# Optimization experiments

Measured on AMD Instinct MI355X. Metric: run time of the kernel, lower is better.

Reference implementation:

```python
import jax, jax.numpy as jnp
import numpy as np

CUTOFF = 5.0
CUTOFF_ANGLE = 3.5
N = 25000
E = 800000
EA = 300000
T = 1600000
NBASIS = 8          # default radial basis size (bessel)
NBASIS_ANG = 8
DIM = 256
DIM_SRC = 64
DIM_DST = 32
DIM_ANGLE = 8
NMAX_ANGLE = 4
SPECIES_DIM = 16
NSPEC = 50


def bessel_basis(r, rc, n):
    # sin(k*pi*r/rc)/r Bessel-type radial basis, k=1..n  -> [E, n]
    x = r[:, None]
    k = jnp.arange(1, n + 1, dtype=r.dtype)[None, :] * (np.pi / rc)
    return jnp.sqrt(2.0 / rc) * jnp.sin(k * x) / x


def tssr2(x):
    # two-sided smooth square-root activation (identity inside |x|<=1)
    ax = jnp.abs(x)
    return jnp.where(ax <= 1.0, x, jnp.sign(x) * (2.0 * jnp.sqrt(jnp.maximum(ax, 1.0)) - 1.0))


def setup_inputs() -> dict:
    key = jax.random.key(0)
    ks = jax.random.split(key, 24)
    species = jax.random.randint(ks[0], (N,), 1, 17)
    edge_src = jax.random.randint(ks[1], (E,), 0, N)
    edge_dst = jax.random.randint(ks[2], (E,), 0, N)
    distances = 0.5 + jax.random.uniform(ks[3], (E,)) * (CUTOFF - 0.5)
    switch = 0.5 + 0.5 * jnp.cos(np.pi * distances / CUTOFF)
    angles = jax.random.uniform(ks[4], (T,)) * np.pi
    angle_src = jax.random.randint(ks[5], (T,), 0, EA)
    angle_dst = jax.random.randint(ks[6], (T,), 0, EA)
    central_atom = jax.random.randint(ks[7], (T,), 0, N)
    distances_angle = 0.5 + jax.random.uniform(ks[8], (EA,)) * (CUTOFF_ANGLE - 0.5)
    switch_angle = 0.5 + 0.5 * jnp.cos(np.pi * distances_angle / CUTOFF_ANGLE)
    s = lambda k, sh, scale: jax.random.normal(k, sh, jnp.float32) * scale
    din0 = SPECIES_DIM + DIM_SRC + NBASIS * DIM_DST + (NMAX_ANGLE + 1) * DIM_ANGLE  # 376
    din1 = DIM + DIM_SRC + NBASIS * DIM_DST + (NMAX_ANGLE + 1) * DIM_ANGLE          # 616
    return {
        'species': species, 'edge_src': edge_src, 'edge_dst': edge_dst,
        'distances': distances, 'switch': switch,
        'angles': angles, 'angle_src': angle_src, 'angle_dst': angle_dst,
        'central_atom': central_atom, 'distances_angle': distances_angle,
        'switch_angle': switch_angle,
        'species_table': s(ks[9], (NSPEC, SPECIES_DIM), 1.0),
        'W_si0': s(ks[10], (SPECIES_DIM, DIM_SRC + DIM_DST), SPECIES_DIM ** -0.5),
        'W_si1': s(ks[11], (DIM, DIM_SRC + DIM_DST), DIM ** -0.5),
        'W_da0': s(ks[12], (NBASIS_ANG, DIM_ANGLE), NBASIS_ANG ** -0.5),
        'W_da1': s(ks[13], (NBASIS_ANG, DIM_ANGLE), NBASIS_ANG ** -0.5),
        'W_mix0': s(ks[14], (din0, DIM), din0 ** -0.5),
        'b_mix0': jnp.zeros((DIM,), jnp.float32),
        'W_mix1': s(ks[15], (din1, DIM), din1 ** -0.5),
        'b_mix1': jnp.zeros((DIM,), jnp.float32),
    }


def reference(species, edge_src, edge_dst, distances, switch, angles, angle_src,
              angle_dst, central_atom, distances_angle, switch_angle,
              species_table, W_si0, W_si1, W_da0, W_da1,
              W_mix0, b_mix0, W_mix1, b_mix1):
    n_atoms = species.shape[0]
    # species encoding (learned/random table lookup)
    xi = species_table[species]                                   # [N, 16]
    # radial embeddings, smoothly switched at cutoff
    rb = bessel_basis(distances, CUTOFF, NBASIS) * switch[:, None]            # [E, 8]
    rba = bessel_basis(distances_angle, CUTOFF_ANGLE, NBASIS_ANG) * switch_angle[:, None]  # [EA, 8]
    # fourier angular features cos(n*theta), n=0..nmax_angle
    nvec = jnp.arange(NMAX_ANGLE + 1, dtype=angles.dtype)[None, :]
    xa = jnp.cos(nvec * angles[:, None])                          # [T, 5]
    for W_si, W_da, W_mix, b_mix in ((W_si0, W_da0, W_mix0, b_mix0),
                                     (W_si1, W_da1, W_mix1, b_mix1)):
        s = xi @ W_si                                             # [N, 96]
        si, si_dst = s[:, :DIM_SRC], s[:, DIM_SRC:]
        # radial message passing: outer(radial_basis, neighbor features) -> scatter-add
        mij = (rb[:, :, None] * si_dst[edge_dst][:, None, :]).reshape(rb.shape[0], -1)  # [E, 256]
        mi = jax.ops.segment_sum(mij, edge_src, num_segments=n_atoms)                   # [N, 256]
        # angular triplet features: pairwise vectors combined per angle
        da = rba @ W_da                                           # [EA, 8]
        dij = da[angle_src] * da[angle_dst]                       # [T, 8]
        ang = (xa[:, :, None] * dij[:, None, :]).reshape(xa.shape[0], -1)               # [T, 40]
        ami = jax.ops.segment_sum(ang, central_atom, num_segments=n_atoms)              # [N, 40]
        # mixing network + tssr2 mixing activation, residual when shapes match
        ei = jnp.concatenate([xi, si, mi, ami], axis=-1)
        dxi = tssr2(ei @ W_mix + b_mix)
        xi = xi + dxi if xi.shape[-1] == dxi.shape[-1] else dxi
    return xi
```

## Files before the change

kernel.cpp:

```cpp
#include <hip/hip_runtime.h>
#include <hip/hip_bf16.h>

typedef __hip_bfloat16 bf16;
typedef __bf16 bf8 __attribute__((ext_vector_type(8)));
typedef float  f4  __attribute__((ext_vector_type(4)));

#define N_ATOMS 25000
#define NE      800000
#define NEA     300000
#define NT      1600000
#define APB     64
#define NBUK    ((N_ATOMS + APB - 1) / APB)

#define DIN0  376
#define DIN1  616
#define DINP0 384
#define DINP1 640

#define EBLK ((NE + 4095) / 4096)

__device__ __forceinline__ float tssr2f(float x) {
    float ax = fabsf(x);
    return (ax <= 1.f) ? x : copysignf(2.f * __builtin_sqrtf(ax) - 1.f, x);
}

__device__ __forceinline__ unsigned short f2bf_rn(float v) {
    unsigned int b = __float_as_uint(v);
    b += 0x7FFF + ((b >> 16) & 1);
    return (unsigned short)(b >> 16);
}
__device__ __forceinline__ float bf2f(unsigned short u) {
    return __uint_as_float(((unsigned int)u) << 16);
}

__global__ __launch_bounds__(256) void k_bcount(const int* __restrict__ esrc,
                                                const int* __restrict__ cat,
                                                int* __restrict__ ebcnt,
                                                int* __restrict__ tbcnt) {
    __shared__ int h[NBUK];
    int t = threadIdx.x;
    for (int b = t; b < NBUK; b += 256) h[b] = 0;
    __syncthreads();
    bool isE = blockIdx.x < EBLK;
    const int* key = isE ? esrc : cat;
    int n = isE ? NE : NT;
    int base = (isE ? blockIdx.x : (blockIdx.x - EBLK)) * 4096;
#pragma unroll
    for (int k = 0; k < 16; k++) {
        int idx = base + k * 256 + t;
        if (idx < n) atomicAdd(&h[key[idx] >> 6], 1);
    }
    __syncthreads();
    int* g = isE ? ebcnt : tbcnt;
    for (int b = t; b < NBUK; b += 256)
        if (h[b]) atomicAdd(&g[b], h[b]);
}

__global__ __launch_bounds__(512) void k_scanB(const int* cnt0, int* off0, int* cur0,
                                               int* aoff0,
                                               const int* cnt1, int* off1, int* cur1,
                                               int* aoff1) {
    const int* cnt = blockIdx.x ? cnt1 : cnt0;
    int* off  = blockIdx.x ? off1 : off0;
    int* cur  = blockIdx.x ? cur1 : cur0;
    int* aoff = blockIdx.x ? aoff1 : aoff0;
    int nelem = blockIdx.x ? NT : NE;
    __shared__ int sh[512];
    int t = threadIdx.x;
    int v = (t < NBUK) ? cnt[t] : 0;
    sh[t] = v;
    __syncthreads();
    for (int d = 1; d < 512; d <<= 1) {
        int a = (t >= d) ? sh[t - d] : 0;
        __syncthreads();
        sh[t] += a;
        __syncthreads();
    }
    int excl = sh[t] - v;
    if (t <= NBUK) { off[t] = excl; if (t < NBUK) cur[t] = excl; }
    if (t == 0) aoff[N_ATOMS] = nelem;
}

template <bool EDGE>
__global__ __launch_bounds__(512) void k_binA(const float* __restrict__ fA,
                                              const float* __restrict__ fB,
                                              const int* __restrict__ iB,
                                              const int* __restrict__ iC,
                                              const int* __restrict__ key,
                                              int* __restrict__ gcur,
                                              float4* __restrict__ buk, int n) {
    __shared__ int cnt[NBUK];
    __shared__ int rbase[NBUK];
    int t = threadIdx.x;
    for (int b = t; b < NBUK; b += 512) cnt[b] = 0;
    __syncthreads();
    int base = blockIdx.x * 4096;
    float4 pay[8];
    int bk[8], off[8];
#pragma unroll
    for (int k = 0; k < 8; k++) {
        int idx = base + k * 512 + t;
        bk[k] = -1;
        if (idx < n) {
            float4 p;
            p.x = EDGE ? fA[idx] : __cosf(fA[idx]);
            p.y = EDGE ? fB[idx] : __int_as_float(iB[idx]);
            p.z = __int_as_float(iC[idx]);
            int ky = key[idx];
            p.w = __int_as_float(ky);
            pay[k] = p;
            bk[k] = ky >> 6;
            off[k] = atomicAdd(&cnt[bk[k]], 1);
        }
    }
    __syncthreads();
    for (int b = t; b < NBUK; b += 512)
        if (cnt[b]) rbase[b] = atomicAdd(&gcur[b], cnt[b]);
    __syncthreads();
#pragma unroll
    for (int k = 0; k < 8; k++)
        if (bk[k] >= 0) buk[rbase[bk[k]] + off[k]] = pay[k];
}

template <bool EDGE>
__global__ __launch_bounds__(256) void k_binB(const int* __restrict__ bkoff,
                                              const float4* __restrict__ buk,
                                              float4* __restrict__ fin,
                                              float* __restrict__ erb,
                                              int* __restrict__ edi,
                                              int* __restrict__ aoff) {
    int b = blockIdx.x;
    int lo = b * APB;
    int hi = min(lo + APB, N_ATOMS);
    __shared__ int cnt[APB];
    __shared__ int cur[APB];
    int t = threadIdx.x;
    if (t < APB) cnt[t] = 0;
    __syncthreads();
    int pbeg = bkoff[b], pend = bkoff[b + 1];
    for (int p = pbeg + t; p < pend; p += 256) {
        int a = __float_as_int(((const float*)(buk + p))[3]);
        atomicAdd(&cnt[a - lo], 1);
    }
    __syncthreads();
    if (t == 0) {
        int run = pbeg;
        for (int k = 0; k < hi - lo; k++) {
            cur[k] = run;
            aoff[lo + k] = run;
            run += cnt[k];
        }
    }
    __syncthreads();
    for (int p = pbeg + t; p < pend; p += 256) {
        float4 pay = buk[p];
        int a = __float_as_int(pay.w);
        int slot = atomicAdd(&cur[a - lo], 1);
        if (EDGE) {
            float d = pay.x, s = pay.y;
            float q = 0.6324555320f * s / d;
            float r[8];
#pragma unroll
            for (int n = 0; n < 8; n++)
                r[n] = q * __sinf((n + 1) * 0.6283185307f * d);
            *(float4*)&erb[(size_t)slot * 8]     = make_float4(r[0], r[1], r[2], r[3]);
            *(float4*)&erb[(size_t)slot * 8 + 4] = make_float4(r[4], r[5], r[6], r[7]);
            edi[slot] = __float_as_int(pay.z);
        } else {
            fin[slot] = pay;
        }
    }
}

__global__ void k_wprep(const float* __restrict__ W, bf8* __restrict__ Wf,
                        int K, int N, int ntiles, int nfrag) {
    int f = blockIdx.x * blockDim.x + threadIdx.x;
    if (f >= nfrag) return;
    int lane = f & 63;
    int ft = f >> 6;
    int tile = ft % ntiles;
    int chunk = ft / ntiles;
    int n = tile * 16 + (lane & 15);
    int kb = chunk * 32 + (lane >> 4) * 8;
    bf8 v;
#pragma unroll
    for (int j = 0; j < 8; j++) {
        int k = kb + j;
        v[j] = (__bf16)((k < K) ? W[k * N + n] : 0.f);
    }
    Wf[f] = v;
}

__global__ void k_s0(const int* __restrict__ sp, const float* __restrict__ table,
                     const float* __restrict__ W, float* __restrict__ ei0,
                     float* __restrict__ sd) {
    int idx = blockIdx.x * blockDim.x + threadIdx.x;
    if (idx >= N_ATOMS * 120) return;
    int i = idx / 120;
    int c = idx - i * 120;
    if (c >= 112) {
        ei0[(size_t)i * DINP0 + 376 + (c - 112)] = 0.f;
        return;
    }
    int s = sp[i];
    if (c < 16) {
        ei0[(size_t)i * DINP0 + c] = table[s * 16 + c];
    } else {
        int cc = c - 16;
        float acc = 0.f;
#pragma unroll
        for (int k = 0; k < 16; k++)
            acc += table[s * 16 + k] * W[k * 96 + cc];
        if (cc < 64) ei0[(size_t)i * DINP0 + 16 + cc] = acc;
        else         sd[i * 32 + cc - 64]             = acc;
    }
}

__global__ __launch_bounds__(256) void k_s1(const float* __restrict__ ei1,
                                            const bf8* __restrict__ Wf,
                                            float* __restrict__ ei1o,
                                            float* __restrict__ sd) {
    __shared__ __align__(16) __bf16 Asg[4][64][8];
    int t = threadIdx.x;
    int w = t >> 6, lane = t & 63;
    int a0 = blockIdx.x * 64;

    int satom = a0 + (t >> 2);
    int k8 = (t & 3) * 8;
    const float* arow = &ei1[(size_t)satom * DINP1 + k8];
    bool aok = satom < N_ATOMS;
    int dw = (t >> 2) >> 4;
    int dl = ((t >> 2) & 15) | ((t & 3) << 4);
    __bf16* adst = &Asg[dw][dl][0];

    f4 acc[6];
#pragma unroll
    for (int j = 0; j < 6; j++) {
        f4 z = {0.f, 0.f, 0.f, 0.f};
        acc[j] = z;
    }

    for (int ch = 0; ch < 8; ch++) {
        float4 v0 = make_float4(0.f, 0.f, 0.f, 0.f);
        float4 v1 = make_float4(0.f, 0.f, 0.f, 0.f);
        if (aok) {
            v0 = *(const float4*)(arow + ch * 32);
            v1 = *(const float4*)(arow + ch * 32 + 4);
        }
        __syncthreads();
        adst[0] = (__bf16)v0.x; adst[1] = (__bf16)v0.y;
        adst[2] = (__bf16)v0.z; adst[3] = (__bf16)v0.w;
        adst[4] = (__bf16)v1.x; adst[5] = (__bf16)v1.y;
        adst[6] = (__bf16)v1.z; adst[7] = (__bf16)v1.w;
        __syncthreads();
        bf8 afr = *(const bf8*)&Asg[w][lane][0];
        const bf8* wp = &Wf[(ch * 6) * 64 + lane];
#pragma unroll
        for (int tn = 0; tn < 6; tn++) {
            bf8 b = wp[tn * 64];
            acc[tn] = __builtin_amdgcn_mfma_f32_16x16x32_bf16(afr, b, acc[tn], 0, 0, 0);
        }
    }

    int nlo = lane & 15, q = lane >> 4;
#pragma unroll
    for (int r = 0; r < 4; r++) {
        int atom = a0 + w * 16 + q * 4 + r;
        if (atom < N_ATOMS) {
#pragma unroll
            for (int tn = 0; tn < 6; tn++) {
                int col = tn * 16 + nlo;
                float v = acc[tn][r];
                if (col < 64) ei1o[(size_t)atom * DINP1 + 256 + col] = v;
                else          sd[atom * 32 + col - 64] = v;
            }
        }
    }
    for (int z = t; z < 64 * 24; z += 256) {
        int za = a0 + z / 24;
        if (za < N_ATOMS) ei1o[(size_t)za * DINP1 + 616 + z % 24] = 0.f;
    }
}

__global__ void k_da(const float* __restrict__ dist, const float* __restrict__ sw,
                     const float* __restrict__ W, unsigned short* __restrict__ dah) {
    int e = blockIdx.x * blockDim.x + threadIdx.x;
    if (e >= NEA) return;
    float d = dist[e];
    float s = sw[e];
    float rb[8];
#pragma unroll
    for (int n = 0; n < 8; n++)
        rb[n] = 0.7559289460f * __sinf((n + 1) * 0.8975979010f * d) / d * s;
    unsigned short h[8];
#pragma unroll
    for (int c = 0; c < 8; c++) {
        float acc = 0.f;
#pragma unroll
        for (int n = 0; n < 8; n++) acc += rb[n] * W[n * 8 + c];
        h[c] = f2bf_rn(acc);
    }
    *(uint4*)&dah[e * 8] = *(uint4*)h;
}

__global__ __launch_bounds__(256) void k_mi(const int* __restrict__ eoff,
                                            const float* __restrict__ erb,
                                            const int* __restrict__ edi,
                                            const float* __restrict__ sd,
                                            float* __restrict__ mo, int stride) {
    int t = threadIdx.x;
    int wv = t >> 6, l = t & 63;
    int slot = wv >> 1;
    int p    = wv & 1;
    int i = blockIdx.x * 2 + slot;
    bool valid = (i < N_ATOMS);
    int beg = 0, end = 0;
    if (valid) { beg = eoff[i]; end = eoff[i + 1]; }
    int cnt = end - beg;
    int n = l >> 3, cb = (l & 7) * 4;
    float4 acc = make_float4(0.f, 0.f, 0.f, 0.f);

    if (cnt > 0) {
        int nG = (cnt + 7) >> 3;
        int h0 = (nG + 1) >> 1;
        int gbeg = p ? h0 : 0;
        int gend = p ? nG : h0;
        if (cnt <= 64) {
            int eWin = edi[beg + min(l, cnt - 1)];
            int cmax = end * 8 - 1;
            for (int g = gbeg; g < gend; g++) {
                int e8 = g * 8;
                float cc = erb[min((beg + e8) * 8 + l, cmax)];
                float4 v[8];
#pragma unroll
                for (int j = 0; j < 8; j++) {
                    int eid = __shfl(eWin, e8 + j, 64);
                    v[j] = *(const float4*)&sd[eid * 32 + cb];
                }
#pragma unroll
                for (int j = 0; j < 8; j++) {
                    float r_ = __shfl(cc, j * 8 + n, 64);
                    r_ = (e8 + j < cnt) ? r_ : 0.f;
                    acc.x += r_ * v[j].x; acc.y += r_ * v[j].y;
                    acc.z += r_ * v[j].z; acc.w += r_ * v[j].w;
                }
            }
        } else {
            const float* rp = erb + (size_t)beg * 8 + n;
            const int*   dp = edi + beg;
            for (int g = gbeg; g < gend; g++) {
                int e8 = g * 8;
                int m = cnt - e8;
#pragma unroll
                for (int j = 0; j < 8; j++) {
                    int jj = min(j, m - 1);
                    float rb = rp[(e8 + jj) * 8];
                    int di = dp[e8 + jj];
                    if (j >= m) rb = 0.f;
                    float4 v = *(const float4*)&sd[di * 32 + cb];
                    acc.x += rb * v.x; acc.y += rb * v.y;
                    acc.z += rb * v.z; acc.w += rb * v.w;
                }
            }
        }
    }

    __shared__ float4 part[2][64];
    if (p == 1) part[slot][l] = acc;
    __syncthreads();
    if (valid && p == 0) {
        float4 o = part[slot][l];
        acc.x += o.x; acc.y += o.y; acc.z += o.z; acc.w += o.w;
        *(float4*)&mo[(size_t)i * stride + l * 4] = acc;
    }
}

__global__ __launch_bounds__(256) void k_ami(const int* __restrict__ toff,
                                             const float4* __restrict__ tpay,
                                             const unsigned short* __restrict__ dah,
                                             float* __restrict__ ao, int stride) {
    int t = threadIdx.x;
    int w = t >> 6, l = t & 63;
    int i = blockIdx.x * 4 + w;
    if (i >= N_ATOMS) return;
    int beg = toff[i], end = toff[i + 1];
    int cnt = end - beg;
    int jj = l >> 3, c = l & 7;
    float a0 = 0.f, a1 = 0.f, a2 = 0.f, a3 = 0.f, a4 = 0.f;

    if (cnt > 0) {
        int nW = (cnt + 63) >> 6;
        float4 twA = tpay[beg + min(l, cnt - 1)];

#define AMI_PREP(SC, DA, DB, g) do {                                       \
        int sl_ = (g) * 8 + jj;                                            \
        SC = __shfl(twA.x, sl_, 64);                                       \
        int ea_ = __float_as_int(__shfl(twA.y, sl_, 64));                  \
        int eb_ = __float_as_int(__shfl(twA.z, sl_, 64));                  \
        DA = dah[ea_ * 8 + c];                                             \
        DB = dah[eb_ * 8 + c];                                             \
    } while (0)

#define AMI_FMAG(SC, DA, DB, g) do {                                       \
        float dij_ = bf2f(DA) * bf2f(DB);                                  \
        dij_ = (wbase + (g) * 8 + jj < cnt) ? dij_ : 0.f;                  \
        float c1_ = SC;                                                    \
        float c2_ = __builtin_fmaf(2.f * c1_, c1_, -1.f);                  \
        float c3_ = __builtin_fmaf(2.f * c1_, c2_, -c1_);                  \
        float c4_ = __builtin_fmaf(2.f * c1_, c3_, -c2_);                  \
        a0 += dij_;                                                        \
        a1 = __builtin_fmaf(c1_, dij_, a1);                                \
        a2 = __builtin_fmaf(c2_, dij_, a2);                                \
        a3 = __builtin_fmaf(c3_, dij_, a3);                                \
        a4 = __builtin_fmaf(c4_, dij_, a4);                                \
    } while (0)

        for (int W = 0; W < nW; W++) {
            int wbase = W * 64;
            float4 twN = twA;
            if (W + 1 < nW) twN = tpay[beg + min(wbase + 64 + l, cnt - 1)];
            int rem = cnt - wbase;
            int gmax = min(8, (rem + 7) >> 3);
            float scA, scB;
            unsigned short daA, dbA, daB, dbB;
            AMI_PREP(scA, daA, dbA, 0);
            int g = 0;
            for (; g + 2 <= gmax; g += 2) {
                AMI_PREP(scB, daB, dbB, g + 1);
                AMI_FMAG(scA, daA, dbA, g);
                if (g + 2 < gmax) AMI_PREP(scA, daA, dbA, g + 2);
                AMI_FMAG(scB, daB, dbB, g + 1);
            }
            if (g < gmax) AMI_FMAG(scA, daA, dbA, g);
            twA = twN;
        }
#undef AMI_PREP
#undef AMI_FMAG
    }

#pragma unroll
    for (int msk = 8; msk <= 32; msk <<= 1) {
        a0 += __shfl_xor(a0, msk, 64);
        a1 += __shfl_xor(a1, msk, 64);
        a2 += __shfl_xor(a2, msk, 64);
        a3 += __shfl_xor(a3, msk, 64);
        a4 += __shfl_xor(a4, msk, 64);
    }
    if (l < 8) {
        float* o = &ao[(size_t)i * stride + c];
        o[0]  = a0;
        o[8]  = a1;
        o[16] = a2;
        o[24] = a3;
        o[32] = a4;
    }
}

template <int LAYER>
__global__ __launch_bounds__(256) void k_gemm(const float* __restrict__ ei,
                                              const bf8* __restrict__ Wf,
                                              const float* __restrict__ bias,
                                              const float* __restrict__ skip,
                                              float* __restrict__ out) {
    constexpr int DINP = (LAYER == 0) ? DINP0 : DINP1;
    constexpr int NCH = DINP / 32;
    __shared__ __align__(16) __bf16 Asg[2][64][8];
    int t = threadIdx.x;
    int w = t >> 6, lane = t & 63;
    int a0 = blockIdx.x * 32;

    int f  = t * 4;
    int tA = f >> 9;
    int al = (f >> 3) & 63;
    int j0 = f & 7;
    int sm = al & 15, sq = al >> 4;
    int ga = a0 + tA * 16 + sm;
    const float* arow = &ei[(size_t)ga * DINP + sq * 8 + j0];
    __bf16* adst = &Asg[0][0][0] + f;
    bool aok = (ga < N_ATOMS);

    f4 acc[2][4];
#pragma unroll
    for (int i = 0; i < 2; i++)
#pragma unroll
        for (int j = 0; j < 4; j++) {
            f4 z = {0.f, 0.f, 0.f, 0.f};
            acc[i][j] = z;
        }

    for (int ch = 0; ch < NCH; ch++) {
        float4 v = make_float4(0.f, 0.f, 0.f, 0.f);
        if (aok) v = *(const float4*)(arow + ch * 32);
        __syncthreads();
        adst[0] = (__bf16)v.x; adst[1] = (__bf16)v.y;
        adst[2] = (__bf16)v.z; adst[3] = (__bf16)v.w;
        __syncthreads();
        bf8 afr0 = *(const bf8*)&Asg[0][lane][0];
        bf8 afr1 = *(const bf8*)&Asg[1][lane][0];
        const bf8* wp = &Wf[(ch * 16 + w * 4) * 64 + lane];
#pragma unroll
        for (int tn = 0; tn < 4; tn++) {
            bf8 b = wp[tn * 64];
            acc[0][tn] = __builtin_amdgcn_mfma_f32_16x16x32_bf16(afr0, b, acc[0][tn], 0, 0, 0);
            acc[1][tn] = __builtin_amdgcn_mfma_f32_16x16x32_bf16(afr1, b, acc[1][tn], 0, 0, 0);
        }
    }

    int nlo = lane & 15, q = lane >> 4;
#pragma unroll
    for (int tA2 = 0; tA2 < 2; tA2++) {
#pragma unroll
        for (int r = 0; r < 4; r++) {
            int atom = a0 + tA2 * 16 + q * 4 + r;
            if (atom < N_ATOMS) {
#pragma unroll
                for (int tn = 0; tn < 4; tn++) {
                    int col = w * 64 + tn * 16 + nlo;
                    float vv = tssr2f(acc[tA2][tn][r] + bias[col]);
                    if (LAYER == 0) {
                        out[(size_t)atom * DINP1 + col] = vv;
                    } else {
                        out[(size_t)atom * 256 + col] = vv + skip[(size_t)atom * DINP1 + col];
                    }
                }
            }
        }
    }
}

extern "C" void kernel_launch(void* const* d_in, const int* in_sizes, int n_in,
                              void* d_out, int out_size, void* d_ws, size_t ws_size,
                              hipStream_t stream) {
    const int*   species     = (const int*)d_in[0];
    const int*   edge_src    = (const int*)d_in[1];
    const int*   edge_dst    = (const int*)d_in[2];
    const float* distances   = (const float*)d_in[3];
    const float* sw          = (const float*)d_in[4];
    const float* angles      = (const float*)d_in[5];
    const int*   angle_src   = (const int*)d_in[6];
    const int*   angle_dst   = (const int*)d_in[7];
    const int*   central     = (const int*)d_in[8];
    const float* dist_a      = (const float*)d_in[9];
    const float* sw_a        = (const float*)d_in[10];
    const float* table       = (const float*)d_in[11];
    const float* W_si0       = (const float*)d_in[12];
    const float* W_si1       = (const float*)d_in[13];
    const float* W_da0       = (const float*)d_in[14];
    const float* W_da1       = (const float*)d_in[15];
    const float* W_mix0      = (const float*)d_in[16];
    const float* b_mix0      = (const float*)d_in[17];
    const float* W_mix1      = (const float*)d_in[18];
    const float* b_mix1      = (const float*)d_in[19];
    float* out = (float*)d_out;

    char* p = (char*)d_ws;
    auto alloc = [&](size_t bytes) {
        char* r = p;
        p += (bytes + 255) & ~(size_t)255;
        return (void*)r;
    };
    float*  ei0  = (float*)alloc((size_t)N_ATOMS * DINP0 * 4);
    float*  ei1  = (float*)alloc((size_t)N_ATOMS * DINP1 * 4);
    float*  sd   = (float*)alloc((size_t)N_ATOMS * 32 * 4);
    unsigned short* dah = (unsigned short*)alloc((size_t)NEA * 8 * 2);
    float*  erbf = (float*)alloc((size_t)NE * 8 * 4);
    int*    edi  = (int*)alloc((size_t)NE * 4);
    float4* tpay = (float4*)alloc((size_t)NT * 16);
    bf8*    Wf0  = (bf8*)alloc((size_t)(DINP0 / 32) * 16 * 64 * 16);
    bf8*    Wf1  = (bf8*)alloc((size_t)(DINP1 / 32) * 16 * 64 * 16);
    bf8*    WfS1 = (bf8*)alloc((size_t)8 * 6 * 64 * 16);
    int* eoff   = (int*)alloc((size_t)(N_ATOMS + 1) * 4);
    int* toff   = (int*)alloc((size_t)(N_ATOMS + 1) * 4);
    int* ebcnt  = (int*)alloc((size_t)NBUK * 4);
    int* tbcnt  = (int*)alloc((size_t)NBUK * 4);
    int* ebkoff = (int*)alloc((size_t)(NBUK + 1) * 4);
    int* tbkoff = (int*)alloc((size_t)(NBUK + 1) * 4);
    int* gce    = (int*)alloc((size_t)NBUK * 4);
    int* gct    = (int*)alloc((size_t)NBUK * 4);
    (void)ws_size;

    float4* tbuk = (float4*)ei1;
    float4* ebuk = (float4*)((char*)ei1 + (size_t)NT * 16);

    hipMemsetAsync(ebcnt, 0, (size_t)NBUK * 4, stream);
    hipMemsetAsync(tbcnt, 0, (size_t)NBUK * 4, stream);

    int nfrag0 = (DINP0 / 32) * 16 * 64;
    int nfrag1 = (DINP1 / 32) * 16 * 64;
    int nfragS = 8 * 6 * 64;
    k_wprep<<<(nfrag0 + 255) / 256, 256, 0, stream>>>(W_mix0, Wf0, DIN0, 256, 16, nfrag0);
    k_wprep<<<(nfrag1 + 255) / 256, 256, 0, stream>>>(W_mix1, Wf1, DIN1, 256, 16, nfrag1);
    k_wprep<<<(nfragS + 255) / 256, 256, 0, stream>>>(W_si1, WfS1, 256, 96, 6, nfragS);

    k_bcount<<<EBLK + (NT + 4095) / 4096, 256, 0, stream>>>(edge_src, central, ebcnt, tbcnt);
    k_scanB<<<2, 512, 0, stream>>>(ebcnt, ebkoff, gce, eoff, tbcnt, tbkoff, gct, toff);

    k_binA<true><<<(NE + 4095) / 4096, 512, 0, stream>>>(
        distances, sw, nullptr, edge_dst, edge_src, gce, ebuk, NE);
    k_binA<false><<<(NT + 4095) / 4096, 512, 0, stream>>>(
        angles, nullptr, angle_src, angle_dst, central, gct, tbuk, NT);
    k_binB<true><<<NBUK, 256, 0, stream>>>(ebkoff, ebuk, nullptr, erbf, edi, eoff);
    k_binB<false><<<NBUK, 256, 0, stream>>>(tbkoff, tbuk, tpay, nullptr, nullptr, toff);

    int gemm_grid = (N_ATOMS + 31) / 32;
    int seg_grid = (N_ATOMS + 3) / 4;
    int mi_grid  = (N_ATOMS + 1) / 2;

    k_s0<<<(N_ATOMS * 120 + 255) / 256, 256, 0, stream>>>(species, table, W_si0, ei0, sd);
    k_da<<<(NEA + 255) / 256, 256, 0, stream>>>(dist_a, sw_a, W_da0, dah);
    k_mi<<<mi_grid, 256, 0, stream>>>(eoff, erbf, edi, sd, ei0 + 80, DINP0);
    k_ami<<<seg_grid, 256, 0, stream>>>(toff, tpay, dah, ei0 + 336, DINP0);
    k_gemm<0><<<gemm_grid, 256, 0, stream>>>(ei0, Wf0, b_mix0, nullptr, ei1);

    k_s1<<<(N_ATOMS + 63) / 64, 256, 0, stream>>>(ei1, WfS1, ei1, sd);
    k_da<<<(NEA + 255) / 256, 256, 0, stream>>>(dist_a, sw_a, W_da1, dah);
    k_mi<<<mi_grid, 256, 0, stream>>>(eoff, erbf, edi, sd, ei1 + 320, DINP1);
    k_ami<<<seg_grid, 256, 0, stream>>>(toff, tpay, dah, ei1 + 576, DINP1);
    k_gemm<1><<<gemm_grid, 256, 0, stream>>>(ei1, Wf1, b_mix1, ei1, out);
}
```

Measured before the change: 440.4 us.

## Merge paired kernels into combined launches to cut launch count

Several pairs of independent kernels become single launches that pick their branch from the block index: the weight prep kernels, the edge and triplet binning passes, species/angle-basis precompute (both layers' angular projections computed at once), and the radial and angular segment sums. The goal is fewer kernel launches and launch gaps, plus better GPU fill for small kernels. The ami path is also restructured so two waves split each atom's triplets and combine through shared memory. In exchange, a second angular buffer is needed and the work per block becomes uneven between branches.

New measurement: 417.6 us. 5.2% less time.

```diff
diff --git a/kernel.cpp b/kernel.cpp
--- a/kernel.cpp
+++ b/kernel.cpp
@@ -18,6 +18,16 @@
 #define DINP1 640
 
 #define EBLK ((NE + 4095) / 4096)
+#define TBLK ((NT + 4095) / 4096)
+
+#define NFRAG0 ((DINP0 / 32) * 16 * 64)
+#define NFRAG1 ((DINP1 / 32) * 16 * 64)
+#define NFRAGS (8 * 6 * 64)
+
+#define S0BLK ((N_ATOMS * 120 + 255) / 256)
+#define DABLK ((NEA + 255) / 256)
+
+#define MIBLK ((N_ATOMS + 1) / 2)
 
 __device__ __forceinline__ float tssr2f(float x) {
     float ax = fabsf(x);
@@ -81,20 +91,29 @@
     if (t == 0) aoff[N_ATOMS] = nelem;
 }
 
-template <bool EDGE>
-__global__ __launch_bounds__(512) void k_binA(const float* __restrict__ fA,
-                                              const float* __restrict__ fB,
-                                              const int* __restrict__ iB,
-                                              const int* __restrict__ iC,
-                                              const int* __restrict__ key,
-                                              int* __restrict__ gcur,
-                                              float4* __restrict__ buk, int n) {
+__global__ __launch_bounds__(512) void k_binA2(const float* __restrict__ eA,
+                                               const float* __restrict__ eB,
+                                               const int* __restrict__ eC,
+                                               const int* __restrict__ ekey,
+                                               int* __restrict__ egcur,
+                                               float4* __restrict__ ebuk,
+                                               const float* __restrict__ tA,
+                                               const int* __restrict__ tB,
+                                               const int* __restrict__ tC,
+                                               const int* __restrict__ tkey,
+                                               int* __restrict__ tgcur,
+                                               float4* __restrict__ tbuk) {
     __shared__ int cnt[NBUK];
     __shared__ int rbase[NBUK];
     int t = threadIdx.x;
     for (int b = t; b < NBUK; b += 512) cnt[b] = 0;
     __syncthreads();
-    int base = blockIdx.x * 4096;
+    bool isE = blockIdx.x < EBLK;
+    const int* key = isE ? ekey : tkey;
+    int n = isE ? NE : NT;
+    int* gcur = isE ? egcur : tgcur;
+    float4* buk = isE ? ebuk : tbuk;
+    int base = (isE ? blockIdx.x : (blockIdx.x - EBLK)) * 4096;
     float4 pay[8];
     int bk[8], off[8];
 #pragma unroll
@@ -103,9 +122,15 @@
         bk[k] = -1;
         if (idx < n) {
             float4 p;
-            p.x = EDGE ? fA[idx] : __cosf(fA[idx]);
-            p.y = EDGE ? fB[idx] : __int_as_float(iB[idx]);
-            p.z = __int_as_float(iC[idx]);
+            if (isE) {
+                p.x = eA[idx];
+                p.y = eB[idx];
+                p.z = __int_as_float(eC[idx]);
+            } else {
+                p.x = __cosf(tA[idx]);
+                p.y = __int_as_float(tB[idx]);
+                p.z = __int_as_float(tC[idx]);
+            }
             int ky = key[idx];
             p.w = __int_as_float(ky);
             pay[k] = p;
@@ -122,14 +147,20 @@
         if (bk[k] >= 0) buk[rbase[bk[k]] + off[k]] = pay[k];
 }
 
-template <bool EDGE>
-__global__ __launch_bounds__(256) void k_binB(const int* __restrict__ bkoff,
-                                              const float4* __restrict__ buk,
-                                              float4* __restrict__ fin,
-                                              float* __restrict__ erb,
-                                              int* __restrict__ edi,
-                                              int* __restrict__ aoff) {
-    int b = blockIdx.x;
+__global__ __launch_bounds__(256) void k_binB2(const int* __restrict__ ebkoff,
+                                               const float4* __restrict__ ebuk,
+                                               float* __restrict__ erb,
+                                               int* __restrict__ edi,
+                                               int* __restrict__ eoff,
+                                               const int* __restrict__ tbkoff,
+                                               const float4* __restrict__ tbuk,
+                                               float4* __restrict__ tfin,
+                                               int* __restrict__ toff) {
+    bool isE = blockIdx.x < NBUK;
+    int b = isE ? blockIdx.x : (blockIdx.x - NBUK);
+    const int* bkoff = isE ? ebkoff : tbkoff;
+    const float4* buk = isE ? ebuk : tbuk;
+    int* aoff = isE ? eoff : toff;
     int lo = b * APB;
     int hi = min(lo + APB, N_ATOMS);
     __shared__ int cnt[APB];
@@ -156,7 +187,7 @@
         float4 pay = buk[p];
         int a = __float_as_int(pay.w);
         int slot = atomicAdd(&cur[a - lo], 1);
-        if (EDGE) {
+        if (isE) {
             float d = pay.x, s = pay.y;
             float q = 0.6324555320f * s / d;
             float r[8];
@@ -167,15 +198,13 @@
             *(float4*)&erb[(size_t)slot * 8 + 4] = make_float4(r[4], r[5], r[6], r[7]);
             edi[slot] = __float_as_int(pay.z);
         } else {
-            fin[slot] = pay;
-        }
-    }
-}
-
-__global__ void k_wprep(const float* __restrict__ W, bf8* __restrict__ Wf,
-                        int K, int N, int ntiles, int nfrag) {
-    int f = blockIdx.x * blockDim.x + threadIdx.x;
-    if (f >= nfrag) return;
+            tfin[slot] = pay;
+        }
+    }
+}
+
+__device__ __forceinline__ void wprep_one(const float* __restrict__ W, bf8* __restrict__ Wf,
+                                          int K, int N, int ntiles, int f) {
     int lane = f & 63;
     int ft = f >> 6;
     int tile = ft % ntiles;
@@ -191,28 +220,74 @@
     Wf[f] = v;
 }
 
-__global__ void k_s0(const int* __restrict__ sp, const float* __restrict__ table,
-                     const float* __restrict__ W, float* __restrict__ ei0,
-                     float* __restrict__ sd) {
-    int idx = blockIdx.x * blockDim.x + threadIdx.x;
-    if (idx >= N_ATOMS * 120) return;
-    int i = idx / 120;
-    int c = idx - i * 120;
-    if (c >= 112) {
-        ei0[(size_t)i * DINP0 + 376 + (c - 112)] = 0.f;
-        return;
-    }
-    int s = sp[i];
-    if (c < 16) {
-        ei0[(size_t)i * DINP0 + c] = table[s * 16 + c];
+__global__ __launch_bounds__(256) void k_wprep3(const float* __restrict__ W0, bf8* __restrict__ Wf0,
+                                                const float* __restrict__ W1, bf8* __restrict__ Wf1,
+                                                const float* __restrict__ WS, bf8* __restrict__ WfS) {
+    int f = blockIdx.x * 256 + threadIdx.x;
+    if (f < NFRAG0) {
+        wprep_one(W0, Wf0, DIN0, 256, 16, f);
+    } else if (f < NFRAG0 + NFRAG1) {
+        wprep_one(W1, Wf1, DIN1, 256, 16, f - NFRAG0);
+    } else if (f < NFRAG0 + NFRAG1 + NFRAGS) {
+        wprep_one(WS, WfS, 256, 96, 6, f - NFRAG0 - NFRAG1);
+    }
+}
+
+__global__ __launch_bounds__(256) void k_pre(const int* __restrict__ sp,
+                                             const float* __restrict__ table,
+                                             const float* __restrict__ W,
+                                             float* __restrict__ ei0,
+                                             float* __restrict__ sd,
+                                             const float* __restrict__ dist,
+                                             const float* __restrict__ sw,
+                                             const float* __restrict__ Wda0,
+                                             const float* __restrict__ Wda1,
+                                             unsigned short* __restrict__ dah0,
+                                             unsigned short* __restrict__ dah1) {
+    if ((int)blockIdx.x < S0BLK) {
+        int idx = blockIdx.x * 256 + threadIdx.x;
+        if (idx >= N_ATOMS * 120) return;
+        int i = idx / 120;
+        int c = idx - i * 120;
+        if (c >= 112) {
+            ei0[(size_t)i * DINP0 + 376 + (c - 112)] = 0.f;
+            return;
+        }
+        int s = sp[i];
+        if (c < 16) {
+            ei0[(size_t)i * DINP0 + c] = table[s * 16 + c];
+        } else {
+            int cc = c - 16;
+            float acc = 0.f;
+#pragma unroll
+            for (int k = 0; k < 16; k++)
+                acc += table[s * 16 + k] * W[k * 96 + cc];
+            if (cc < 64) ei0[(size_t)i * DINP0 + 16 + cc] = acc;
+            else         sd[i * 32 + cc - 64]             = acc;
+        }
     } else {
-        int cc = c - 16;
-        float acc = 0.f;
-#pragma unroll
-        for (int k = 0; k < 16; k++)
-            acc += table[s * 16 + k] * W[k * 96 + cc];
-        if (cc < 64) ei0[(size_t)i * DINP0 + 16 + cc] = acc;
-        else         sd[i * 32 + cc - 64]             = acc;
+        int e = (blockIdx.x - S0BLK) * 256 + threadIdx.x;
+        if (e >= NEA) return;
+        float d = dist[e];
+        float s = sw[e];
+        float rb[8];
+#pragma unroll
+        for (int n = 0; n < 8; n++)
+            rb[n] = 0.7559289460f * __sinf((n + 1) * 0.8975979010f * d) / d * s;
+        unsigned short h0[8], h1[8];
+#pragma unroll
+        for (int c = 0; c < 8; c++) {
+            float a0 = 0.f, a1 = 0.f;
+#pragma unroll
+            for (int n = 0; n < 8; n++) {
+                a0 += rb[n] * Wda0[n * 8 + c];
+                a1 += rb[n] * Wda1[n * 8 + c];
+            }
+            h0[c] = f2bf_rn(a0);
+            h1[c] = f2bf_rn(a1);
+        }
+        *(uint4*)&dah0[e * 8] = *(uint4*)h0;
+        *(uint4*)&dah1[e * 8] = *(uint4*)h1;
     }
 }
 
@@ -282,177 +357,180 @@
     }
 }
 
-__global__ void k_da(const float* __restrict__ dist, const float* __restrict__ sw,
-                     const float* __restrict__ W, unsigned short* __restrict__ dah) {
-    int e = blockIdx.x * blockDim.x + threadIdx.x;
-    if (e >= NEA) return;
-    float d = dist[e];
-    float s = sw[e];
-    float rb[8];
-#pragma unroll
-    for (int n = 0; n < 8; n++)
-        rb[n] = 0.7559289460f * __sinf((n + 1) * 0.8975979010f * d) / d * s;
-    unsigned short h[8];
-#pragma unroll
-    for (int c = 0; c < 8; c++) {
-        float acc = 0.f;
-#pragma unroll
-        for (int n = 0; n < 8; n++) acc += rb[n] * W[n * 8 + c];
-        h[c] = f2bf_rn(acc);
-    }
-    *(uint4*)&dah[e * 8] = *(uint4*)h;
-}
-
-__global__ __launch_bounds__(256) void k_mi(const int* __restrict__ eoff,
-                                            const float* __restrict__ erb,
-                                            const int* __restrict__ edi,
-                                            const float* __restrict__ sd,
-                                            float* __restrict__ mo, int stride) {
+__device__ __forceinline__ void ami_win(const float4 twA, const unsigned short* __restrict__ dah,
+                                        int lim, int jj, int c,
+                                        float& a0, float& a1, float& a2, float& a3, float& a4) {
+    int gmax = (lim + 7) >> 3;
+    float sc = 0.f; unsigned short dA = 0, dB = 0;
+    {
+        sc = __shfl(twA.x, jj, 64);
+        int ea = __float_as_int(__shfl(twA.y, jj, 64));
+        int eb = __float_as_int(__shfl(twA.z, jj, 64));
+        dA = dah[ea * 8 + c];
+        dB = dah[eb * 8 + c];
+    }
+    for (int g = 0; g < gmax; g++) {
+        float scN = 0.f; unsigned short dAN = 0, dBN = 0;
+        if (g + 1 < gmax) {
+            int sl = (g + 1) * 8 + jj;
+            scN = __shfl(twA.x, sl, 64);
+            int ea = __float_as_int(__shfl(twA.y, sl, 64));
+            int eb = __float_as_int(__shfl(twA.z, sl, 64));
+            dAN = dah[ea * 8 + c];
+            dBN = dah[eb * 8 + c];
+        }
+        float dij = bf2f(dA) * bf2f(dB);
+        dij = (g * 8 + jj < lim) ? dij : 0.f;
+        float c1 = sc;
+        float c2 = __builtin_fmaf(2.f * c1, c1, -1.f);
+        float c3 = __builtin_fmaf(2.f * c1, c2, -c1);
+        float c4 = __builtin_fmaf(2.f * c1, c3, -c2);
+        a0 += dij;
+        a1 = __builtin_fmaf(c1, dij, a1);
+        a2 = __builtin_fmaf(c2, dij, a2);
+        a3 = __builtin_fmaf(c3, dij, a3);
+        a4 = __builtin_fmaf(c4, dij, a4);
+        if (g + 1 < gmax) { sc = scN; dA = dAN; dB = dBN; }
+    }
+}
+
+__global__ __launch_bounds__(256) void k_seg(const int* __restrict__ eoff,
+                                             const float* __restrict__ erb,
+                                             const int* __restrict__ edi,
+                                             const float* __restrict__ sd,
+                                             float* __restrict__ mo, int mstride,
+                                             const int* __restrict__ toff,
+                                             const float4* __restrict__ tpay,
+                                             const unsigned short* __restrict__ dah,
+                                             float* __restrict__ ao, int astride) {
+    __shared__ float4 smi[2][64];
+    __shared__ float  sam[2][5][8];
     int t = threadIdx.x;
     int wv = t >> 6, l = t & 63;
     int slot = wv >> 1;
     int p    = wv & 1;
-    int i = blockIdx.x * 2 + slot;
-    bool valid = (i < N_ATOMS);
-    int beg = 0, end = 0;
-    if (valid) { beg = eoff[i]; end = eoff[i + 1]; }
-    int cnt = end - beg;
-    int n = l >> 3, cb = (l & 7) * 4;
-    float4 acc = make_float4(0.f, 0.f, 0.f, 0.f);
-
-    if (cnt > 0) {
-        int nG = (cnt + 7) >> 3;
-        int h0 = (nG + 1) >> 1;
-        int gbeg = p ? h0 : 0;
-        int gend = p ? nG : h0;
-        if (cnt <= 64) {
-            int eWin = edi[beg + min(l, cnt - 1)];
-            int cmax = end * 8 - 1;
-            for (int g = gbeg; g < gend; g++) {
-                int e8 = g * 8;
-                float cc = erb[min((beg + e8) * 8 + l, cmax)];
-                float4 v[8];
-#pragma unroll
-                for (int j = 0; j < 8; j++) {
-                    int eid = __shfl(eWin, e8 + j, 64);
-                    v[j] = *(const float4*)&sd[eid * 32 + cb];
+
+    if ((int)blockIdx.x < MIBLK) {
+        int i = blockIdx.x * 2 + slot;
+        bool valid = (i < N_ATOMS);
+        int beg = 0, end = 0;
+        if (valid) { beg = eoff[i]; end = eoff[i + 1]; }
+        int cnt = end - beg;
+        int n = l >> 3, cb = (l & 7) * 4;
+        float4 acc = make_float4(0.f, 0.f, 0.f, 0.f);
+
+        if (cnt > 0) {
+            int nG = (cnt + 7) >> 3;
+            int h0 = (nG + 1) >> 1;
+            int gbeg = p ? h0 : 0;
+            int gend = p ? nG : h0;
+            if (cnt <= 64) {
+                int eWin = edi[beg + min(l, cnt - 1)];
+                int cmax = end * 8 - 1;
+                if (gbeg < gend) {
+                    float cA = erb[min((beg + gbeg * 8) * 8 + l, cmax)];
+                    for (int g = gbeg; g < gend; g++) {
+                        int e8 = g * 8;
+                        float4 v[8];
+#pragma unroll
+                        for (int j = 0; j < 8; j++) {
+                            int eid = __shfl(eWin, e8 + j, 64);
+                            v[j] = *(const float4*)&sd[eid * 32 + cb];
+                        }
+                        float cB = 0.f;
+                        if (g + 1 < gend) cB = erb[min((beg + e8 + 8) * 8 + l, cmax)];
+#pragma unroll
+                        for (int j = 0; j < 8; j++) {
+                            float r_ = __shfl(cA, j * 8 + n, 64);
+                            r_ = (e8 + j < cnt) ? r_ : 0.f;
+                            acc.x += r_ * v[j].x; acc.y += r_ * v[j].y;
+                            acc.z += r_ * v[j].z; acc.w += r_ * v[j].w;
+                        }
+                        if (g + 1 < gend) cA = cB;
+                    }
                 }
-#pragma unroll
-                for (int j = 0; j < 8; j++) {
-                    float r_ = __shfl(cc, j * 8 + n, 64);
-                    r_ = (e8 + j < cnt) ? r_ : 0.f;
-                    acc.x += r_ * v[j].x; acc.y += r_ * v[j].y;
-                    acc.z += r_ * v[j].z; acc.w += r_ * v[j].w;
+            } else {
+                const float* rp = erb + (size_t)beg * 8 + n;
+                const int*   dp = edi + beg;
+                for (int g = gbeg; g < gend; g++) {
+                    int e8 = g * 8;
+                    int m = cnt - e8;
+#pragma unroll
+                    for (int j = 0; j < 8; j++) {
+                        int jj = min(j, m - 1);
+                        float rb = rp[(e8 + jj) * 8];
+                        int di = dp[e8 + jj];
+                        if (j >= m) rb = 0.f;
+                        float4 v = *(const float4*)&sd[di * 32 + cb];
+                        acc.x += rb * v.x; acc.y += rb * v.y;
+                        acc.z += rb * v.z; acc.w += rb * v.w;
+                    }
                 }
             }
-        } else {
-            const float* rp = erb + (size_t)beg * 8 + n;
-            const int*   dp = edi + beg;
-            for (int g = gbeg; g < gend; g++) {
-                int e8 = g * 8;
-                int m = cnt - e8;
-#pragma unroll
-                for (int j = 0; j < 8; j++) {
-                    int jj = min(j, m - 1);
-                    float rb = rp[(e8 + jj) * 8];
-                    int di = dp[e8 + jj];
-                    if (j >= m) rb = 0.f;
-                    float4 v = *(const float4*)&sd[di * 32 + cb];
-                    acc.x += rb * v.x; acc.y += rb * v.y;
-                    acc.z += rb * v.z; acc.w += rb * v.w;
+        }
+
+        if (p == 1) smi[slot][l] = acc;
+        __syncthreads();
+        if (valid && p == 0) {
+            float4 o = smi[slot][l];
+            acc.x += o.x; acc.y += o.y; acc.z += o.z; acc.w += o.w;
+            *(float4*)&mo[(size_t)i * mstride + l * 4] = acc;
+        }
+    } else {
+        int i = ((int)blockIdx.x - MIBLK) * 2 + slot;
+        bool valid = (i < N_ATOMS);
+        int beg = 0, end = 0;
+        if (valid) { beg = toff[i]; end = toff[i + 1]; }
+        int cnt = end - beg;
+        int jj = l >> 3, c = l & 7;
+        float a0 = 0.f, a1 = 0.f, a2 = 0.f, a3 = 0.f, a4 = 0.f;
+
+        if (cnt > 0) {
+            if (cnt <= 128) {
+                int nG = (cnt + 7) >> 3;
+                int h0 = (nG + 1) >> 1;
+                int tb = p ? h0 * 8 : 0;
+                int te = p ? cnt : min(h0 * 8, cnt);
+                int mycnt = te - tb;
+                if (mycnt > 0) {
+                    float4 twA = tpay[beg + tb + min(l, mycnt - 1)];
+                    ami_win(twA, dah, mycnt, jj, c, a0, a1, a2, a3, a4);
+                }
+            } else {
+                int nW = (cnt + 63) >> 6;
+                for (int W = p; W < nW; W += 2) {
+                    int wbase = W * 64;
+                    int rem = cnt - wbase;
+                    int lim = min(rem, 64);
+                    float4 twA = tpay[beg + wbase + min(l, rem - 1)];
+                    ami_win(twA, dah, lim, jj, c, a0, a1, a2, a3, a4);
                 }
             }
         }
-    }
-
-    __shared__ float4 part[2][64];
-    if (p == 1) part[slot][l] = acc;
-    __syncthreads();
-    if (valid && p == 0) {
-        float4 o = part[slot][l];
-        acc.x += o.x; acc.y += o.y; acc.z += o.z; acc.w += o.w;
-        *(float4*)&mo[(size_t)i * stride + l * 4] = acc;
-    }
-}
-
-__global__ __launch_bounds__(256) void k_ami(const int* __restrict__ toff,
-                                             const float4* __restrict__ tpay,
-                                             const unsigned short* __restrict__ dah,
-                                             float* __restrict__ ao, int stride) {
-    int t = threadIdx.x;
-    int w = t >> 6, l = t & 63;
-    int i = blockIdx.x * 4 + w;
-    if (i >= N_ATOMS) return;
-    int beg = toff[i], end = toff[i + 1];
-    int cnt = end - beg;
-    int jj = l >> 3, c = l & 7;
-    float a0 = 0.f, a1 = 0.f, a2 = 0.f, a3 = 0.f, a4 = 0.f;
-
-    if (cnt > 0) {
-        int nW = (cnt + 63) >> 6;
-        float4 twA = tpay[beg + min(l, cnt - 1)];
-
-#define AMI_PREP(SC, DA, DB, g) do {                                       \
-        int sl_ = (g) * 8 + jj;                                            \
-        SC = __shfl(twA.x, sl_, 64);                                       \
-        int ea_ = __float_as_int(__shfl(twA.y, sl_, 64));                  \
-        int eb_ = __float_as_int(__shfl(twA.z, sl_, 64));                  \
-        DA = dah[ea_ * 8 + c];                                             \
-        DB = dah[eb_ * 8 + c];                                             \
-    } while (0)
-
-#define AMI_FMAG(SC, DA, DB, g) do {                                       \
-        float dij_ = bf2f(DA) * bf2f(DB);                                  \
-        dij_ = (wbase + (g) * 8 + jj < cnt) ? dij_ : 0.f;                  \
-        float c1_ = SC;                                                    \
-        float c2_ = __builtin_fmaf(2.f * c1_, c1_, -1.f);                  \
-        float c3_ = __builtin_fmaf(2.f * c1_, c2_, -c1_);                  \
-        float c4_ = __builtin_fmaf(2.f * c1_, c3_, -c2_);                  \
-        a0 += dij_;                                                        \
-        a1 = __builtin_fmaf(c1_, dij_, a1);                                \
-        a2 = __builtin_fmaf(c2_, dij_, a2);                                \
-        a3 = __builtin_fmaf(c3_, dij_, a3);                                \
-        a4 = __builtin_fmaf(c4_, dij_, a4);                                \
-    } while (0)
-
-        for (int W = 0; W < nW; W++) {
-            int wbase = W * 64;
-            float4 twN = twA;
-            if (W + 1 < nW) twN = tpay[beg + min(wbase + 64 + l, cnt - 1)];
-            int rem = cnt - wbase;
-            int gmax = min(8, (rem + 7) >> 3);
-            float scA, scB;
-            unsigned short daA, dbA, daB, dbB;
-            AMI_PREP(scA, daA, dbA, 0);
-            int g = 0;
-            for (; g + 2 <= gmax; g += 2) {
-                AMI_PREP(scB, daB, dbB, g + 1);
-                AMI_FMAG(scA, daA, dbA, g);
-                if (g + 2 < gmax) AMI_PREP(scA, daA, dbA, g + 2);
-                AMI_FMAG(scB, daB, dbB, g + 1);
-            }
-            if (g < gmax) AMI_FMAG(scA, daA, dbA, g);
-            twA = twN;
-        }
-#undef AMI_PREP
-#undef AMI_FMAG
-    }
-
-#pragma unroll
-    for (int msk = 8; msk <= 32; msk <<= 1) {
-        a0 += __shfl_xor(a0, msk, 64);
-        a1 += __shfl_xor(a1, msk, 64);
-        a2 += __shfl_xor(a2, msk, 64);
-        a3 += __shfl_xor(a3, msk, 64);
-        a4 += __shfl_xor(a4, msk, 64);
-    }
-    if (l < 8) {
-        float* o = &ao[(size_t)i * stride + c];
-        o[0]  = a0;
-        o[8]  = a1;
-        o[16] = a2;
-        o[24] = a3;
-        o[32] = a4;
+
+#pragma unroll
+        for (int msk = 8; msk <= 32; msk <<= 1) {
+            a0 += __shfl_xor(a0, msk, 64);
+            a1 += __shfl_xor(a1, msk, 64);
+            a2 += __shfl_xor(a2, msk, 64);
+            a3 += __shfl_xor(a3, msk, 64);
+            a4 += __shfl_xor(a4, msk, 64);
+        }
+        if (p == 1 && l < 8) {
+            sam[slot][0][l] = a0; sam[slot][1][l] = a1; sam[slot][2][l] = a2;
+            sam[slot][3][l] = a3; sam[slot][4][l] = a4;
+        }
+        __syncthreads();
+        if (valid && p == 0 && l < 8) {
+            a0 += sam[slot][0][l]; a1 += sam[slot][1][l]; a2 += sam[slot][2][l];
+            a3 += sam[slot][3][l]; a4 += sam[slot][4][l];
+            float* o = &ao[(size_t)i * astride + c];
+            o[0]  = a0;
+            o[8]  = a1;
+            o[16] = a2;
+            o[24] = a3;
+            o[32] = a4;
+        }
     }
 }
 
@@ -562,59 +640,55 @@
     float*  ei0  = (float*)alloc((size_t)N_ATOMS * DINP0 * 4);
     float*  ei1  = (float*)alloc((size_t)N_ATOMS * DINP1 * 4);
     float*  sd   = (float*)alloc((size_t)N_ATOMS * 32 * 4);
-    unsigned short* dah = (unsigned short*)alloc((size_t)NEA * 8 * 2);
+    unsigned short* dah0 = (unsigned short*)alloc((size_t)NEA * 8 * 2);
+    unsigned short* dah1 = (unsigned short*)alloc((size_t)NEA * 8 * 2);
     float*  erbf = (float*)alloc((size_t)NE * 8 * 4);
     int*    edi  = (int*)alloc((size_t)NE * 4);
     float4* tpay = (float4*)alloc((size_t)NT * 16);
-    bf8*    Wf0  = (bf8*)alloc((size_t)(DINP0 / 32) * 16 * 64 * 16);
-    bf8*    Wf1  = (bf8*)alloc((size_t)(DINP1 / 32) * 16 * 64 * 16);
-    bf8*    WfS1 = (bf8*)alloc((size_t)8 * 6 * 64 * 16);
+    bf8*    Wf0  = (bf8*)alloc((size_t)NFRAG0 * 16);
+    bf8*    Wf1  = (bf8*)alloc((size_t)NFRAG1 * 16);
+    bf8*    WfS1 = (bf8*)alloc((size_t)NFRAGS * 16);
     int* eoff   = (int*)alloc((size_t)(N_ATOMS + 1) * 4);
     int* toff   = (int*)alloc((size_t)(N_ATOMS + 1) * 4);
-    int* ebcnt  = (int*)alloc((size_t)NBUK * 4);
-    int* tbcnt  = (int*)alloc((size_t)NBUK * 4);
+    int* bcnt   = (int*)alloc((size_t)2 * NBUK * 4);
     int* ebkoff = (int*)alloc((size_t)(NBUK + 1) * 4);
     int* tbkoff = (int*)alloc((size_t)(NBUK + 1) * 4);
     int* gce    = (int*)alloc((size_t)NBUK * 4);
     int* gct    = (int*)alloc((size_t)NBUK * 4);
     (void)ws_size;
+    int* ebcnt = bcnt;
+    int* tbcnt = bcnt + NBUK;
 
     float4* tbuk = (float4*)ei1;
     float4* ebuk = (float4*)((char*)ei1 + (size_t)NT * 16);
 
-    hipMemsetAsync(ebcnt, 0, (size_t)NBUK * 4, stream);
-    hipMemsetAsync(tbcnt, 0, (size_t)NBUK * 4, stream);
-
-    int nfrag0 = (DINP0 / 32) * 16 * 64;
-    int nfrag1 = (DINP1 / 32) * 16 * 64;
-    int nfragS = 8 * 6 * 64;
-    k_wprep<<<(nfrag0 + 255) / 256, 256, 0, stream>>>(W_mix0, Wf0, DIN0, 256, 16, nfrag0);
-    k_wprep<<<(nfrag1 + 255) / 256, 256, 0, stream>>>(W_mix1, Wf1, DIN1, 256, 16, nfrag1);
-    k_wprep<<<(nfragS + 255) / 256, 256, 0, stream>>>(W_si1, WfS1, 256, 96, 6, nfragS);
-
-    k_bcount<<<EBLK + (NT + 4095) / 4096, 256, 0, stream>>>(edge_src, central, ebcnt, tbcnt);
+    hipMemsetAsync(bcnt, 0, (size_t)2 * NBUK * 4, stream);
+
+    k_wprep3<<<(NFRAG0 + NFRAG1 + NFRAGS + 255) / 256, 256, 0, stream>>>(
+        W_mix0, Wf0, W_mix1, Wf1, W_si1, WfS1);
+
+    k_bcount<<<EBLK + TBLK, 256, 0, stream>>>(edge_src, central, ebcnt, tbcnt);
     k_scanB<<<2, 512, 0, stream>>>(ebcnt, ebkoff, gce, eoff, tbcnt, tbkoff, gct, toff);
 
-    k_binA<true><<<(NE + 4095) / 4096, 512, 0, stream>>>(
-        distances, sw, nullptr, edge_dst, edge_src, gce, ebuk, NE);
-    k_binA<false><<<(NT + 4095) / 4096, 512, 0, stream>>>(
-        angles, nullptr, angle_src, angle_dst, central, gct, tbuk, NT);
-    k_binB<true><<<NBUK, 256, 0, stream>>>(ebkoff, ebuk, nullptr, erbf, edi, eoff);
-    k_binB<false><<<NBUK, 256, 0, stream>>>(tbkoff, tbuk, tpay, nullptr, nullptr, toff);
+    k_binA2<<<EBLK + TBLK, 512, 0, stream>>>(
+        distances, sw, edge_dst, edge_src, gce, ebuk,
+        angles, angle_src, angle_dst, central, gct, tbuk);
+    k_binB2<<<2 * NBUK, 256, 0, stream>>>(
+        ebkoff, ebuk, erbf, edi, eoff,
+        tbkoff, tbuk, tpay, toff);
+
+    k_pre<<<S0BLK + DABLK, 256, 0, stream>>>(
+        species, table, W_si0, ei0, sd,
+        dist_a, sw_a, W_da0, W_da1, dah0, dah1);
 
     int gemm_grid = (N_ATOMS + 31) / 32;
-    int seg_grid = (N_ATOMS + 3) / 4;
-    int mi_grid  = (N_ATOMS + 1) / 2;
-
-    k_s0<<<(N_ATOMS * 120 + 255) / 256, 256, 0, stream>>>(species, table, W_si0, ei0, sd);
-    k_da<<<(NEA + 255) / 256, 256, 0, stream>>>(dist_a, sw_a, W_da0, dah);
-    k_mi<<<mi_grid, 256, 0, stream>>>(eoff, erbf, edi, sd, ei0 + 80, DINP0);
-    k_ami<<<seg_grid, 256, 0, stream>>>(toff, tpay, dah, ei0 + 336, DINP0);
+
+    k_seg<<<2 * MIBLK, 256, 0, stream>>>(eoff, erbf, edi, sd, ei0 + 80, DINP0,
+                                         toff, tpay, dah0, ei0 + 336, DINP0);
     k_gemm<0><<<gemm_grid, 256, 0, stream>>>(ei0, Wf0, b_mix0, nullptr, ei1);
 
     k_s1<<<(N_ATOMS + 63) / 64, 256, 0, stream>>>(ei1, WfS1, ei1, sd);
-    k_da<<<(NEA + 255) / 256, 256, 0, stream>>>(dist_a, sw_a, W_da1, dah);
-    k_mi<<<mi_grid, 256, 0, stream>>>(eoff, erbf, edi, sd, ei1 + 320, DINP1);
-    k_ami<<<seg_grid, 256, 0, stream>>>(toff, tpay, dah, ei1 + 576, DINP1);
+    k_seg<<<2 * MIBLK, 256, 0, stream>>>(eoff, erbf, edi, sd, ei1 + 320, DINP1,
+                                         toff, tpay, dah1, ei1 + 576, DINP1);
     k_gemm<1><<<gemm_grid, 256, 0, stream>>>(ei1, Wf1, b_mix1, ei1, out);
 }
```
